# Kernel tuning notes

Hardware: AMD Instinct MI355X
Metric: run time of the kernel (lower is better)

The kernel has to match this reference:

```python
import jax, jax.numpy as jnp
import numpy as np

N_NODES = 100000
N_EDGES = 1600000
N_FEAT = 128
HIDDEN = 128
N_GRAPHS = 64
N_CLASSES = 10
BN_EPS = 1e-5


def setup_inputs() -> dict:
    key = jax.random.key(0)
    ks = jax.random.split(key, 24)
    glorot = lambda k, o, i: jax.random.normal(k, (o, i), jnp.float32) * (1.0 / np.sqrt(i))
    inp = {
        'x': jax.random.normal(ks[0], (N_NODES, N_FEAT), jnp.float32),
        'edge_index': jax.random.randint(ks[1], (2, N_EDGES), 0, N_NODES, jnp.int64),
        'batch': jnp.sort(jax.random.randint(ks[2], (N_NODES,), 0, N_GRAPHS, jnp.int64)),
        # GCNConv(128 -> 128)
        'gcn_w': glorot(ks[3], HIDDEN, N_FEAT),
        'gcn_b': jnp.zeros((HIDDEN,), jnp.float32),
        # SAGEConv layers 1, 2: lin_l (aggregated, with bias) + lin_r (root, no bias)
        'sage1_wl': glorot(ks[4], HIDDEN, HIDDEN),
        'sage1_bl': jnp.zeros((HIDDEN,), jnp.float32),
        'sage1_wr': glorot(ks[5], HIDDEN, HIDDEN),
        'sage2_wl': glorot(ks[6], HIDDEN, HIDDEN),
        'sage2_bl': jnp.zeros((HIDDEN,), jnp.float32),
        'sage2_wr': glorot(ks[7], HIDDEN, HIDDEN),
        # ClassifierBase: 128 -> 200 -> 100 -> 50 -> 10
        'clf_w0': glorot(ks[8], 200, HIDDEN), 'clf_b0': jnp.zeros((200,), jnp.float32),
        'clf_w1': glorot(ks[9], 100, 200), 'clf_b1': jnp.zeros((100,), jnp.float32),
        'clf_w2': glorot(ks[10], 50, 100), 'clf_b2': jnp.zeros((50,), jnp.float32),
        'clf_w3': glorot(ks[11], N_CLASSES, 50), 'clf_b3': jnp.zeros((N_CLASSES,), jnp.float32),
        # BatchNorm1d (eval mode, running_mean=0, running_var=1)
        'bn0_g': jnp.ones((200,), jnp.float32), 'bn0_b': jnp.zeros((200,), jnp.float32),
        'bn1_g': jnp.ones((100,), jnp.float32), 'bn1_b': jnp.zeros((100,), jnp.float32),
        'bn2_g': jnp.ones((50,), jnp.float32), 'bn2_b': jnp.zeros((50,), jnp.float32),
    }
    return inp


def _gcn_conv(x, src, dst, W, b):
    # PyG GCNConv: add self loops, symmetric deg^{-1/2} normalization
    xw = x @ W.T                                                  # [N, H]
    ones = jnp.ones(src.shape[0], xw.dtype)
    deg = jax.ops.segment_sum(ones, dst, num_segments=N_NODES) + 1.0  # self loops
    dinv = jax.lax.rsqrt(deg)
    norm = dinv[src] * dinv[dst]                                  # [E]
    out = jax.ops.segment_sum(xw[src] * norm[:, None], dst, num_segments=N_NODES)
    out = out + xw * (dinv * dinv)[:, None]                       # self-loop term deg^{-1}
    return out + b


def _sage_conv(x, src, dst, Wl, bl, Wr):
    # PyG SAGEConv (mean aggr): lin_l(mean_{j->i} x_j) + lin_r(x_i)
    ones = jnp.ones(src.shape[0], x.dtype)
    cnt = jax.ops.segment_sum(ones, dst, num_segments=N_NODES)
    agg = jax.ops.segment_sum(x[src], dst, num_segments=N_NODES)
    agg = agg / jnp.maximum(cnt, 1.0)[:, None]
    return agg @ Wl.T + bl + x @ Wr.T


def _bn_eval(h, g, b):
    # eval-mode BatchNorm1d with running_mean=0, running_var=1
    return h * (g / np.sqrt(1.0 + BN_EPS)) + b


def reference(x, edge_index, batch, gcn_w, gcn_b,
              sage1_wl, sage1_bl, sage1_wr, sage2_wl, sage2_bl, sage2_wr,
              clf_w0, clf_b0, clf_w1, clf_b1, clf_w2, clf_b2, clf_w3, clf_b3,
              bn0_g, bn0_b, bn1_g, bn1_b, bn2_g, bn2_b):
    src, dst = edge_index[0], edge_index[1]
    h = _gcn_conv(x, src, dst, gcn_w, gcn_b)          # act_func is None -> no activation
    h = _sage_conv(h, src, dst, sage1_wl, sage1_bl, sage1_wr)
    h = _sage_conv(h, src, dst, sage2_wl, sage2_bl, sage2_wr)
    # global mean pool over graphs
    gcnt = jax.ops.segment_sum(jnp.ones(h.shape[0], h.dtype), batch, num_segments=N_GRAPHS)
    g = jax.ops.segment_sum(h, batch, num_segments=N_GRAPHS) / jnp.maximum(gcnt, 1.0)[:, None]
    # ClassifierBase (eval: dropout inactive), tanh activation
    g = jnp.tanh(_bn_eval(g @ clf_w0.T + clf_b0, bn0_g, bn0_b))
    g = jnp.tanh(_bn_eval(g @ clf_w1.T + clf_b1, bn1_g, bn1_b))
    g = jnp.tanh(_bn_eval(g @ clf_w2.T + clf_b2, bn2_g, bn2_b))
    logits = g @ clf_w3.T + clf_b3
    return jax.nn.softmax(logits, axis=1)             # [B, n_classes]
```

## Files before the change

### kernel.cpp

```cpp
#include <hip/hip_runtime.h>

#define N_NODES 100000
#define N_EDGES 1600000
#define NGRAPH 64
#define NBIN 391
#define EPB 6400
#define NBLK 250
#define CAPB 6144
#define CAP 8192
#define PSPLIT 8

typedef short s8v __attribute__((ext_vector_type(8)));
typedef float f4v __attribute__((ext_vector_type(4)));

__device__ __forceinline__ float bflo(unsigned u) { return __uint_as_float(u << 16); }
__device__ __forceinline__ float bfhi(unsigned u) { return __uint_as_float(u & 0xffff0000u); }
__device__ __forceinline__ unsigned short f2bf(float f) {
    unsigned u = __float_as_uint(f);
    u += 0x7fffu + ((u >> 16) & 1u);
    return (unsigned short)(u >> 16);
}
__device__ __forceinline__ float bf2f(unsigned short h) { return __uint_as_float(((unsigned)h) << 16); }
__device__ __forceinline__ unsigned pk(float lo, float hi) {
    return (unsigned)f2bf(lo) | ((unsigned)f2bf(hi) << 16);
}
__device__ __forceinline__ float ldv(const void* p, int i, int f32) {
    return f32 ? ((const float*)p)[i] : bf2f(((const unsigned short*)p)[i]);
}

__global__ void k_detect(const unsigned short* __restrict__ x, const int* __restrict__ ei,
                         const int* __restrict__ batch, int* __restrict__ flags) {
    __shared__ int cnt[3];
    int tid = threadIdx.x;
    if (tid < 3) cnt[tid] = 0;
    __syncthreads();
    unsigned short h = x[tid * 37];
    int e = (h >> 7) & 0xFF;
    if (e >= 100 && e <= 150) atomicAdd(&cnt[0], 1);
    if (ei[2 * (tid * 5000) + 1] == 0) atomicAdd(&cnt[1], 1);
    if (batch[2 * (tid * 193) + 1] == 0) atomicAdd(&cnt[2], 1);
    __syncthreads();
    if (tid == 0) {
        flags[0] = (cnt[0] == 256) ? 0 : 1;
        flags[1] = (cnt[1] == 256) ? 1 : 0;
        flags[2] = (cnt[2] == 256) ? 1 : 0;
    }
}


__global__ void k_bininit(int* __restrict__ binCur) {
    int i = blockIdx.x * 256 + threadIdx.x;
    if (i < NBIN) binCur[i] = i * CAPB;
}

__global__ __launch_bounds__(256) void k_binfill(const int* __restrict__ ei,
                                                 int* __restrict__ binCur,
                                                 unsigned* __restrict__ staging,
                                                 const int* __restrict__ flags) {
    __shared__ int cnt[NBIN];
    __shared__ int lofs[NBIN];
    __shared__ int curL[NBIN];
    __shared__ int basg[NBIN];
    __shared__ int sA[512], sB[512];
    __shared__ unsigned ebuf[EPB];
    int tid = threadIdx.x;
    int i64 = flags[1];
    int base = blockIdx.x * EPB;
    for (int i = tid; i < NBIN; i += 256) cnt[i] = 0;
    __syncthreads();
    for (int k = 0; k < EPB / 256; ++k) {
        int e = base + k * 256 + tid;
        int d = i64 ? ei[2 * (N_EDGES + e)] : ei[N_EDGES + e];
        if ((unsigned)d < N_NODES) atomicAdd(&cnt[d >> 8], 1);
    }
    __syncthreads();
    for (int k = tid; k < 512; k += 256) sA[k] = (k < NBIN) ? cnt[k] : 0;
    __syncthreads();
    int* src = sA;
    int* dst = sB;
    for (int off = 1; off < 512; off <<= 1) {
        for (int k = tid; k < 512; k += 256)
            dst[k] = src[k] + ((k >= off) ? src[k - off] : 0);
        __syncthreads();
        int* t = src; src = dst; dst = t;
    }
    for (int i = tid; i < NBIN; i += 256) {
        int excl = src[i] - cnt[i];
        lofs[i] = excl;
        curL[i] = excl;
        basg[i] = cnt[i] ? atomicAdd(&binCur[i], cnt[i]) : 0;
    }
    __syncthreads();
    for (int k = 0; k < EPB / 256; ++k) {
        int e = base + k * 256 + tid;
        int s = i64 ? ei[2 * e] : ei[e];
        int d = i64 ? ei[2 * (N_EDGES + e)] : ei[N_EDGES + e];
        if ((unsigned)d < N_NODES) {
            s = min(max(s, 0), N_NODES - 1);
            int p = atomicAdd(&curL[d >> 8], 1);
            ebuf[p] = ((unsigned)(d & 255) << 20) | (unsigned)s;
        }
    }
    __syncthreads();
    int wid = tid >> 6, lane = tid & 63;
    for (int b = wid; b < NBIN; b += 4) {
        int n = cnt[b], lo = lofs[b], go = basg[b];
        int cap = (b + 1) * CAPB;
        for (int l = lane; l < n; l += 64)
            if (go + l < cap) staging[go + l] = ebuf[lo + l];
    }
}

__global__ __launch_bounds__(256) void k_csr(const unsigned* __restrict__ staging,
                                             const int* __restrict__ binCur,
                                             int* __restrict__ rsA, int* __restrict__ reA,
                                             float* __restrict__ dinv,
                                             int* __restrict__ colidx) {
    __shared__ int deg[256];
    __shared__ int s[256];
    __shared__ int cur[256];
    __shared__ unsigned ebuf[CAP];
    __shared__ int colbuf[CAP];
    int b = blockIdx.x, tid = threadIdx.x;
    int n0 = b << 8;
    int nend = min(256, N_NODES - n0);
    int runStart = b * CAPB;
    int runLen = min(binCur[b] - runStart, CAPB);
    deg[tid] = 0;
    __syncthreads();
    for (int i = tid; i < runLen; i += 256) {
        unsigned e = staging[runStart + i];
        ebuf[i] = e;
        atomicAdd(&deg[e >> 20], 1);
    }
    __syncthreads();
    int myDeg = deg[tid];
    s[tid] = myDeg;
    __syncthreads();
    for (int off = 1; off < 256; off <<= 1) {
        int x = (tid >= off) ? s[tid - off] : 0;
        __syncthreads();
        s[tid] += x;
        __syncthreads();
    }
    int incl = s[tid];
    if (tid < nend) {
        rsA[n0 + tid] = runStart + incl - myDeg;
        reA[n0 + tid] = runStart + incl;
        dinv[n0 + tid] = rsqrtf((float)myDeg + 1.0f);
    }
    cur[tid] = incl - myDeg;
    __syncthreads();
    for (int i = tid; i < runLen; i += 256) {
        unsigned e = ebuf[i];
        int p = atomicAdd(&cur[e >> 20], 1);
        colbuf[p] = (int)(e & 0xFFFFF);
    }
    __syncthreads();
    for (int i = tid; i < runLen; i += 256) colidx[runStart + i] = colbuf[i];
}

__global__ void k_gb(const int* __restrict__ batch, int* __restrict__ gstart,
                     const int* __restrict__ flags) {
    int g = threadIdx.x;
    if (g > NGRAPH) return;
    int b64 = flags[2];
    int lo = 0, hi = N_NODES;
    while (lo < hi) {
        int mid = (lo + hi) >> 1;
        int v = b64 ? batch[2 * mid] : batch[mid];
        if (v < g) lo = mid + 1;
        else hi = mid;
    }
    gstart[g] = lo;
}

__global__ __launch_bounds__(256) void k_prescale(const void* __restrict__ src,
                                                  const float* __restrict__ dinv,
                                                  unsigned* __restrict__ out,
                                                  const int* __restrict__ flags) {
    int id = blockIdx.x * 256 + threadIdx.x;
    int node = id >> 6;
    float di = dinv[node];
    float lo, hi;
    if (flags[0]) {
        float2 u = ((const float2*)src)[id];
        lo = u.x; hi = u.y;
    } else {
        unsigned u = ((const unsigned*)src)[id];
        lo = bflo(u); hi = bfhi(u);
    }
    out[id] = pk(di * lo, di * hi);
}

__global__ __launch_bounds__(256) void k_agg(const uint4* __restrict__ xs,
                                             const int* __restrict__ rsA,
                                             const int* __restrict__ reA,
                                             const float* __restrict__ dinv,
                                             unsigned* __restrict__ out, int mode,
                                             const int* __restrict__ col) {
    int lane = threadIdx.x & 63;
    int node = blockIdx.x * 4 + (threadIdx.x >> 6);
    int glane = lane & 15, grp = lane >> 4;
    int rs = rsA[node], re = reA[node];
    int deg = re - rs;
    float a[8];
    #pragma unroll
    for (int i = 0; i < 8; ++i) a[i] = 0.f;
    uint4 selfu = make_uint4(0u, 0u, 0u, 0u);
    if (mode == 0) selfu = xs[(size_t)node * 16 + glane];

    int efull = rs + (deg & ~15);
    for (int base = rs; base < efull; base += 16) {
        int j0 = col[base + grp * 4 + 0];
        int j1 = col[base + grp * 4 + 1];
        int j2 = col[base + grp * 4 + 2];
        int j3 = col[base + grp * 4 + 3];
        uint4 u0 = xs[(size_t)j0 * 16 + glane];
        uint4 u1 = xs[(size_t)j1 * 16 + glane];
        uint4 u2 = xs[(size_t)j2 * 16 + glane];
        uint4 u3 = xs[(size_t)j3 * 16 + glane];
        a[0] += bflo(u0.x) + bflo(u1.x) + bflo(u2.x) + bflo(u3.x);
        a[1] += bfhi(u0.x) + bfhi(u1.x) + bfhi(u2.x) + bfhi(u3.x);
        a[2] += bflo(u0.y) + bflo(u1.y) + bflo(u2.y) + bflo(u3.y);
        a[3] += bfhi(u0.y) + bfhi(u1.y) + bfhi(u2.y) + bfhi(u3.y);
        a[4] += bflo(u0.z) + bflo(u1.z) + bflo(u2.z) + bflo(u3.z);
        a[5] += bfhi(u0.z) + bfhi(u1.z) + bfhi(u2.z) + bfhi(u3.z);
        a[6] += bflo(u0.w) + bflo(u1.w) + bflo(u2.w) + bflo(u3.w);
        a[7] += bfhi(u0.w) + bfhi(u1.w) + bfhi(u2.w) + bfhi(u3.w);
    }
    if (efull < re) {
        int j[4];
        float w[4];
        #pragma unroll
        for (int k = 0; k < 4; ++k) {
            int ee = efull + grp * 4 + k;
            bool v = ee < re;
            j[k] = col[v ? ee : re - 1];
            w[k] = v ? 1.f : 0.f;
        }
        uint4 u0 = xs[(size_t)j[0] * 16 + glane];
        uint4 u1 = xs[(size_t)j[1] * 16 + glane];
        uint4 u2 = xs[(size_t)j[2] * 16 + glane];
        uint4 u3 = xs[(size_t)j[3] * 16 + glane];
        a[0] += w[0] * bflo(u0.x) + w[1] * bflo(u1.x) + w[2] * bflo(u2.x) + w[3] * bflo(u3.x);
        a[1] += w[0] * bfhi(u0.x) + w[1] * bfhi(u1.x) + w[2] * bfhi(u2.x) + w[3] * bfhi(u3.x);
        a[2] += w[0] * bflo(u0.y) + w[1] * bflo(u1.y) + w[2] * bflo(u2.y) + w[3] * bflo(u3.y);
        a[3] += w[0] * bfhi(u0.y) + w[1] * bfhi(u1.y) + w[2] * bfhi(u2.y) + w[3] * bfhi(u3.y);
        a[4] += w[0] * bflo(u0.z) + w[1] * bflo(u1.z) + w[2] * bflo(u2.z) + w[3] * bflo(u3.z);
        a[5] += w[0] * bfhi(u0.z) + w[1] * bfhi(u1.z) + w[2] * bfhi(u2.z) + w[3] * bfhi(u3.z);
        a[6] += w[0] * bflo(u0.w) + w[1] * bflo(u1.w) + w[2] * bflo(u2.w) + w[3] * bflo(u3.w);
        a[7] += w[0] * bfhi(u0.w) + w[1] * bfhi(u1.w) + w[2] * bfhi(u2.w) + w[3] * bfhi(u3.w);
    }
    #pragma unroll
    for (int i = 0; i < 8; ++i) {
        float v = a[i];
        v += __shfl_xor(v, 16, 64);
        v += __shfl_xor(v, 32, 64);
        a[i] = v;
    }
    if (mode == 0) {
        float di = dinv[node];
        a[0] = di * (a[0] + bflo(selfu.x)); a[1] = di * (a[1] + bfhi(selfu.x));
        a[2] = di * (a[2] + bflo(selfu.y)); a[3] = di * (a[3] + bfhi(selfu.y));
        a[4] = di * (a[4] + bflo(selfu.z)); a[5] = di * (a[5] + bfhi(selfu.z));
        a[6] = di * (a[6] + bflo(selfu.w)); a[7] = di * (a[7] + bfhi(selfu.w));
    } else {
        float s = 1.0f / fmaxf((float)deg, 1.0f);
        #pragma unroll
        for (int i = 0; i < 8; ++i) a[i] *= s;
    }
    if (grp == 0) {
        uint4 o;
        o.x = pk(a[0], a[1]); o.y = pk(a[2], a[3]);
        o.z = pk(a[4], a[5]); o.w = pk(a[6], a[7]);
        *(uint4*)(out + (size_t)node * 64 + glane * 4) = o;
    }
}

template <int DUAL>
__global__ __launch_bounds__(256) void k_gemm(const unsigned short* A0,
                                              const void* __restrict__ W0,
                                              const unsigned short* __restrict__ A1,
                                              const void* __restrict__ W1,
                                              const void* __restrict__ bias,
                                              unsigned short* out,
                                              const int* __restrict__ flags) {
    __shared__ __align__(16) unsigned short As[64][136];
    __shared__ __align__(16) unsigned short Ws[128][136];
    int f32 = flags[0];
    int tid = threadIdx.x;
    int lane = tid & 63;
    int rowbase = blockIdx.x * 64;
    int lr = lane & 15, q = lane >> 4;
    int m0 = (tid >> 6) * 16;

    f4v acc[8];
    #pragma unroll
    for (int t = 0; t < 8; ++t) acc[t] = (f4v){0.f, 0.f, 0.f, 0.f};

    #pragma unroll
    for (int p = 0; p < (DUAL ? 2 : 1); ++p) {
        const unsigned short* Ap = p ? A1 : A0;
        const void* Wp = p ? W1 : W0;
        if (p) __syncthreads();
        #pragma unroll
        for (int it = 0; it < 4; ++it) {
            int chunk = tid + it * 256;
            int r = chunk >> 4, c8 = (chunk & 15) * 8;
            int grow = rowbase + r;
            uint4 v = make_uint4(0u, 0u, 0u, 0u);
            if (grow < N_NODES) v = *(const uint4*)(Ap + (size_t)grow * 128 + c8);
            *(uint4*)&As[r][c8] = v;
        }
        if (!f32) {
            const unsigned short* Wf = (const unsigned short*)Wp;
            #pragma unroll
            for (int it = 0; it < 8; ++it) {
                int chunk = tid + it * 256;
                int r = chunk >> 4, c8 = (chunk & 15) * 8;
                *(uint4*)&Ws[r][c8] = *(const uint4*)(Wf + r * 128 + c8);
            }
        } else {
            const float* Wf = (const float*)Wp;
            #pragma unroll
            for (int it = 0; it < 16; ++it) {
                int chunk = tid + it * 256;
                int r = chunk >> 5, c4 = (chunk & 31) * 4;
                float4 v = *(const float4*)(Wf + r * 128 + c4);
                unsigned lo = (unsigned)f2bf(v.x) | ((unsigned)f2bf(v.y) << 16);
                unsigned hi = (unsigned)f2bf(v.z) | ((unsigned)f2bf(v.w) << 16);
                *(uint2*)&Ws[r][c4] = make_uint2(lo, hi);
            }
        }
        __syncthreads();
        #pragma unroll
        for (int k = 0; k < 4; ++k) {
            s8v a = *(const s8v*)&As[m0 + lr][k * 32 + q * 8];
            #pragma unroll
            for (int t = 0; t < 8; ++t) {
                s8v b = *(const s8v*)&Ws[t * 16 + lr][k * 32 + q * 8];
                acc[t] = __builtin_amdgcn_mfma_f32_16x16x32_bf16(a, b, acc[t], 0, 0, 0);
            }
        }
    }
    #pragma unroll
    for (int t = 0; t < 8; ++t) {
        int o = t * 16 + lr;
        float bv = ldv(bias, o, f32);
        #pragma unroll
        for (int j = 0; j < 4; ++j) {
            int m = rowbase + m0 + q * 4 + j;
            if (m < N_NODES) out[(size_t)m * 128 + o] = f2bf(acc[t][j] + bv);
        }
    }
}

__global__ __launch_bounds__(256) void k_pool2(const unsigned* __restrict__ h,
                                               const int* __restrict__ gstart,
                                               float* __restrict__ ppool) {
    __shared__ float part[4][128];
    int g = blockIdx.x / PSPLIT, sl = blockIdx.x % PSPLIT;
    int wave = threadIdx.x >> 6, lane = threadIdx.x & 63;
    int s0 = gstart[g], s1 = gstart[g + 1];
    int n = s1 - s0;
    int chunk = (n + PSPLIT - 1) / PSPLIT;
    int r0 = s0 + sl * chunk;
    int r1 = min(r0 + chunk, s1);
    float a0 = 0.f, a1 = 0.f;
    for (int r = r0 + wave; r < r1; r += 4) {
        unsigned u = h[(size_t)r * 64 + lane];
        a0 += bflo(u);
        a1 += bfhi(u);
    }
    part[wave][2 * lane] = a0;
    part[wave][2 * lane + 1] = a1;
    __syncthreads();
    int t = threadIdx.x;
    if (t < 128) {
        float s = part[0][t] + part[1][t] + part[2][t] + part[3][t];
        ppool[(size_t)blockIdx.x * 128 + t] = s;
    }
}

__global__ void k_cvt_w(const void* w0, const void* w1, const void* w2, const void* w3,
                        float* __restrict__ wbuf, const int* __restrict__ flags) {
    int f = flags[0];
    int i = blockIdx.x * 256 + threadIdx.x;
    if (i < 25600) wbuf[i] = ldv(w0, i, f);
    else if (i < 45600) wbuf[i] = ldv(w1, i - 25600, f);
    else if (i < 50600) wbuf[i] = ldv(w2, i - 45600, f);
    else if (i < 51100) wbuf[i] = ldv(w3, i - 50600, f);
}

__global__ void k_cvt_p(const void* b0, const void* bn0g, const void* bn0b,
                        const void* b1, const void* bn1g, const void* bn1b,
                        const void* b2, const void* bn2g, const void* bn2b,
                        const void* b3, float* __restrict__ pbuf,
                        const int* __restrict__ flags) {
    int f = flags[0];
    int t = threadIdx.x;
    const float invs = rsqrtf(1.0f + 1e-5f);
    if (t < 200) {
        float a = ldv(bn0g, t, f) * invs;
        pbuf[t] = a;
        pbuf[200 + t] = ldv(b0, t, f) * a + ldv(bn0b, t, f);
    }
    if (t < 100) {
        float a = ldv(bn1g, t, f) * invs;
        pbuf[400 + t] = a;
        pbuf[500 + t] = ldv(b1, t, f) * a + ldv(bn1b, t, f);
    }
    if (t < 50) {
        float a = ldv(bn2g, t, f) * invs;
        pbuf[600 + t] = a;
        pbuf[650 + t] = ldv(b2, t, f) * a + ldv(bn2b, t, f);
    }
    if (t < 10) pbuf[700 + t] = ldv(b3, t, f);
}

__global__ __launch_bounds__(256) void k_clf0(const float* __restrict__ ppool,
                                              const int* __restrict__ gstart,
                                              const float* __restrict__ wbuf,
                                              const float* __restrict__ pbuf,
                                              float* __restrict__ h1) {
    __shared__ float g[128];
    int b = blockIdx.x, t = threadIdx.x;
    if (t < 128) {
        float s = 0.f;
        #pragma unroll
        for (int k = 0; k < PSPLIT; ++k) s += ppool[(size_t)(b * PSPLIT + k) * 128 + t];
        int cnt = gstart[b + 1] - gstart[b];
        g[t] = s / fmaxf((float)cnt, 1.0f);
    }
    __syncthreads();
    if (t < 200) {
        const float4* wr = (const float4*)(wbuf + t * 128);
        float s = 0.f;
        #pragma unroll
        for (int k = 0; k < 32; ++k) {
            float4 v = wr[k];
            s += v.x * g[4 * k] + v.y * g[4 * k + 1] + v.z * g[4 * k + 2] + v.w * g[4 * k + 3];
        }
        h1[b * 200 + t] = tanhf(s * pbuf[t] + pbuf[200 + t]);
    }
}

__global__ __launch_bounds__(128) void k_clf1(const float* __restrict__ h1,
                                              const float* __restrict__ wbuf,
                                              const float* __restrict__ pbuf,
                                              float* __restrict__ h2) {
    __shared__ float g[200];
    int b = blockIdx.x, t = threadIdx.x;
    for (int i = t; i < 200; i += 128) g[i] = h1[b * 200 + i];
    __syncthreads();
    if (t < 100) {
        const float4* wr = (const float4*)(wbuf + 25600 + t * 200);
        float s = 0.f;
        #pragma unroll
        for (int k = 0; k < 50; ++k) {
            float4 v = wr[k];
            s += v.x * g[4 * k] + v.y * g[4 * k + 1] + v.z * g[4 * k + 2] + v.w * g[4 * k + 3];
        }
        h2[b * 100 + t] = tanhf(s * pbuf[400 + t] + pbuf[500 + t]);
    }
}

__global__ __launch_bounds__(128) void k_clf2(const float* __restrict__ h2,
                                              const float* __restrict__ wbuf,
                                              const float* __restrict__ pbuf,
                                              float* __restrict__ h3) {
    __shared__ float g[100];
    int b = blockIdx.x, t = threadIdx.x;
    if (t < 100) g[t] = h2[b * 100 + t];
    __syncthreads();
    if (t < 50) {
        const float4* wr = (const float4*)(wbuf + 45600 + t * 100);
        float s = 0.f;
        #pragma unroll
        for (int k = 0; k < 25; ++k) {
            float4 v = wr[k];
            s += v.x * g[4 * k] + v.y * g[4 * k + 1] + v.z * g[4 * k + 2] + v.w * g[4 * k + 3];
        }
        h3[b * 50 + t] = tanhf(s * pbuf[600 + t] + pbuf[650 + t]);
    }
}

__global__ __launch_bounds__(64) void k_clf3(const float* __restrict__ h3,
                                             const float* __restrict__ wbuf,
                                             const float* __restrict__ pbuf,
                                             void* outv, const int* __restrict__ flags) {
    int b = threadIdx.x;
    int f = flags[0];
    const float* h = h3 + b * 50;
    float lg[10];
    float mx = -1e30f;
    #pragma unroll
    for (int c = 0; c < 10; ++c) {
        const float* wr = wbuf + 50600 + c * 50;
        float s = 0.f;
        for (int k = 0; k < 50; ++k) s += wr[k] * h[k];
        s += pbuf[700 + c];
        lg[c] = s;
        mx = fmaxf(mx, s);
    }
    float sum = 0.f;
    #pragma unroll
    for (int c = 0; c < 10; ++c) {
        lg[c] = __expf(lg[c] - mx);
        sum += lg[c];
    }
    float inv = 1.0f / sum;
    #pragma unroll
    for (int c = 0; c < 10; ++c) {
        float v = lg[c] * inv;
        if (f) ((float*)outv)[b * 10 + c] = v;
        else ((unsigned short*)outv)[b * 10 + c] = f2bf(v);
    }
}

extern "C" void kernel_launch(void* const* d_in, const int* in_sizes, int n_in,
                              void* d_out, int out_size, void* d_ws, size_t ws_size,
                              hipStream_t stream) {
    const unsigned short* x16 = (const unsigned short*)d_in[0];
    const int* ei = (const int*)d_in[1];
    const int* batch = (const int*)d_in[2];

    char* ws = (char*)d_ws;
    size_t off = 0;
    auto alloc = [&](size_t bytes) {
        size_t r = off;
        off = (off + bytes + 255) & ~(size_t)255;
        return r;
    };
    int* flags = (int*)(ws + alloc(256));
    int* rsA = (int*)(ws + alloc((size_t)N_NODES * 4));
    int* reA = (int*)(ws + alloc((size_t)N_NODES * 4));
    int* colidx = (int*)(ws + alloc((size_t)NBIN * CAPB * 4));
    float* dinv = (float*)(ws + alloc((size_t)N_NODES * 4));
    int* binCur = (int*)(ws + alloc(NBIN * 4));
    int* gstart = (int*)(ws + alloc((NGRAPH + 1) * 4));
    float* ppool = (float*)(ws + alloc((size_t)NGRAPH * PSPLIT * 128 * 4));
    float* wbuf = (float*)(ws + alloc(51100 * 4));
    float* pbuf = (float*)(ws + alloc(710 * 4));
    float* h1 = (float*)(ws + alloc(64 * 200 * 4));
    float* h2 = (float*)(ws + alloc(64 * 100 * 4));
    float* h3 = (float*)(ws + alloc(64 * 50 * 4));
    unsigned short* bufA = (unsigned short*)(ws + alloc((size_t)N_NODES * 128 * 2));
    unsigned short* bufB = (unsigned short*)(ws + alloc((size_t)N_NODES * 128 * 2));
    unsigned* staging = (unsigned*)bufA;

    k_detect<<<1, 256, 0, stream>>>(x16, ei, batch, flags);
    k_bininit<<<(NBIN + 255) / 256, 256, 0, stream>>>(binCur);

    k_cvt_w<<<200, 256, 0, stream>>>(d_in[11], d_in[13], d_in[15], d_in[17], wbuf, flags);
    k_cvt_p<<<1, 256, 0, stream>>>(d_in[12], d_in[19], d_in[20], d_in[14], d_in[21], d_in[22],
                                   d_in[16], d_in[23], d_in[24], d_in[18], pbuf, flags);
    k_gb<<<1, 128, 0, stream>>>(batch, gstart, flags);

    k_binfill<<<NBLK, 256, 0, stream>>>(ei, binCur, staging, flags);
    k_csr<<<NBIN, 256, 0, stream>>>(staging, binCur, rsA, reA, dinv, colidx);

    k_prescale<<<N_NODES * 64 / 256, 256, 0, stream>>>((const void*)x16, dinv,
                                                       (unsigned*)bufB, flags);
    k_agg<<<N_NODES / 4, 256, 0, stream>>>((const uint4*)bufB, rsA, reA, dinv,
                                           (unsigned*)bufA, 0, colidx);
    k_gemm<0><<<(N_NODES + 63) / 64, 256, 0, stream>>>(bufA, d_in[3], nullptr, nullptr, d_in[4],
                                                       bufA, flags);
    k_agg<<<N_NODES / 4, 256, 0, stream>>>((const uint4*)bufA, rsA, reA, dinv,
                                           (unsigned*)bufB, 1, colidx);
    k_gemm<1><<<(N_NODES + 63) / 64, 256, 0, stream>>>(bufB, d_in[5], bufA, d_in[7], d_in[6],
                                                       bufB, flags);
    k_agg<<<N_NODES / 4, 256, 0, stream>>>((const uint4*)bufB, rsA, reA, dinv,
                                           (unsigned*)bufA, 1, colidx);
    k_gemm<1><<<(N_NODES + 63) / 64, 256, 0, stream>>>(bufA, d_in[8], bufB, d_in[10], d_in[9],
                                                       bufA, flags);
    k_pool2<<<NGRAPH * PSPLIT, 256, 0, stream>>>((const unsigned*)bufA, gstart, ppool);
    k_clf0<<<NGRAPH, 256, 0, stream>>>(ppool, gstart, wbuf, pbuf, h1);
    k_clf1<<<NGRAPH, 128, 0, stream>>>(h1, wbuf, pbuf, h2);
    k_clf2<<<NGRAPH, 128, 0, stream>>>(h2, wbuf, pbuf, h3);
    k_clf3<<<1, 64, 0, stream>>>(h3, wbuf, pbuf, d_out, flags);
}
```

Before: 524.4 us.

## Fuse setup kernels, fold prescale into CSR, merge pooling with classifier

Result: slower. 568.9 us (+8.5%).

```diff
diff --git a/kernel.cpp b/kernel.cpp
--- a/kernel.cpp
+++ b/kernel.cpp
@@ -28,8 +28,17 @@
     return f32 ? ((const float*)p)[i] : bf2f(((const unsigned short*)p)[i]);
 }
 
-__global__ void k_detect(const unsigned short* __restrict__ x, const int* __restrict__ ei,
-                         const int* __restrict__ batch, int* __restrict__ flags) {
+__global__ __launch_bounds__(256) void k_setup(const unsigned short* __restrict__ x,
+                                               const int* __restrict__ ei,
+                                               const int* __restrict__ batch,
+                                               int* __restrict__ flags,
+                                               int* __restrict__ binCur,
+                                               int* __restrict__ gstart,
+                                               float* __restrict__ pbuf,
+                                               const void* b0, const void* bn0g, const void* bn0b,
+                                               const void* b1, const void* bn1g, const void* bn1b,
+                                               const void* b2, const void* bn2g, const void* bn2b,
+                                               const void* b3) {
     __shared__ int cnt[3];
     int tid = threadIdx.x;
     if (tid < 3) cnt[tid] = 0;
@@ -40,17 +49,41 @@
     if (ei[2 * (tid * 5000) + 1] == 0) atomicAdd(&cnt[1], 1);
     if (batch[2 * (tid * 193) + 1] == 0) atomicAdd(&cnt[2], 1);
     __syncthreads();
+    int f = (cnt[0] == 256) ? 0 : 1;
+    int b64 = (cnt[2] == 256) ? 1 : 0;
     if (tid == 0) {
-        flags[0] = (cnt[0] == 256) ? 0 : 1;
+        flags[0] = f;
         flags[1] = (cnt[1] == 256) ? 1 : 0;
-        flags[2] = (cnt[2] == 256) ? 1 : 0;
-    }
-}
-
-
-__global__ void k_bininit(int* __restrict__ binCur) {
-    int i = blockIdx.x * 256 + threadIdx.x;
-    if (i < NBIN) binCur[i] = i * CAPB;
+        flags[2] = b64;
+    }
+    for (int i = tid; i < NBIN; i += 256) binCur[i] = i * CAPB;
+    if (tid <= NGRAPH) {
+        int g = tid, lo = 0, hi = N_NODES;
+        while (lo < hi) {
+            int mid = (lo + hi) >> 1;
+            int v = b64 ? batch[2 * mid] : batch[mid];
+            if (v < g) lo = mid + 1;
+            else hi = mid;
+        }
+        gstart[g] = lo;
+    }
+    const float invs = rsqrtf(1.0f + 1e-5f);
+    if (tid < 200) {
+        float a = ldv(bn0g, tid, f) * invs;
+        pbuf[tid] = a;
+        pbuf[200 + tid] = ldv(b0, tid, f) * a + ldv(bn0b, tid, f);
+    }
+    if (tid < 100) {
+        float a = ldv(bn1g, tid, f) * invs;
+        pbuf[400 + tid] = a;
+        pbuf[500 + tid] = ldv(b1, tid, f) * a + ldv(bn1b, tid, f);
+    }
+    if (tid < 50) {
+        float a = ldv(bn2g, tid, f) * invs;
+        pbuf[600 + tid] = a;
+        pbuf[650 + tid] = ldv(b2, tid, f) * a + ldv(bn2b, tid, f);
+    }
+    if (tid < 10) pbuf[700 + tid] = ldv(b3, tid, f);
 }
 
 __global__ __launch_bounds__(256) void k_binfill(const int* __restrict__ ei,
@@ -115,7 +148,10 @@
                                              const int* __restrict__ binCur,
                                              int* __restrict__ rsA, int* __restrict__ reA,
                                              float* __restrict__ dinv,
-                                             int* __restrict__ colidx) {
+                                             int* __restrict__ colidx,
+                                             const void* __restrict__ x,
+                                             unsigned* __restrict__ ybuf,
+                                             const int* __restrict__ flags) {
     __shared__ int deg[256];
     __shared__ int s[256];
     __shared__ int cur[256];
@@ -138,9 +174,9 @@
     s[tid] = myDeg;
     __syncthreads();
     for (int off = 1; off < 256; off <<= 1) {
-        int x = (tid >= off) ? s[tid - off] : 0;
+        int x2 = (tid >= off) ? s[tid - off] : 0;
         __syncthreads();
-        s[tid] += x;
+        s[tid] += x2;
         __syncthreads();
     }
     int incl = s[tid];
@@ -158,39 +194,24 @@
     }
     __syncthreads();
     for (int i = tid; i < runLen; i += 256) colidx[runStart + i] = colbuf[i];
-}
-
-__global__ void k_gb(const int* __restrict__ batch, int* __restrict__ gstart,
-                     const int* __restrict__ flags) {
-    int g = threadIdx.x;
-    if (g > NGRAPH) return;
-    int b64 = flags[2];
-    int lo = 0, hi = N_NODES;
-    while (lo < hi) {
-        int mid = (lo + hi) >> 1;
-        int v = b64 ? batch[2 * mid] : batch[mid];
-        if (v < g) lo = mid + 1;
-        else hi = mid;
-    }
-    gstart[g] = lo;
-}
-
-__global__ __launch_bounds__(256) void k_prescale(const void* __restrict__ src,
-                                                  const float* __restrict__ dinv,
-                                                  unsigned* __restrict__ out,
-                                                  const int* __restrict__ flags) {
-    int id = blockIdx.x * 256 + threadIdx.x;
-    int node = id >> 6;
-    float di = dinv[node];
-    float lo, hi;
-    if (flags[0]) {
-        float2 u = ((const float2*)src)[id];
-        lo = u.x; hi = u.y;
-    } else {
-        unsigned u = ((const unsigned*)src)[id];
-        lo = bflo(u); hi = bfhi(u);
-    }
-    out[id] = pk(di * lo, di * hi);
+    int f32 = flags[0];
+    int prow = tid >> 6, ppair = tid & 63;
+    for (int it = 0; it < 64; ++it) {
+        int rl = it * 4 + prow;
+        int r = n0 + rl;
+        if (r < N_NODES) {
+            float di = rsqrtf((float)deg[rl] + 1.0f);
+            float lo, hi;
+            if (f32) {
+                float2 u = ((const float2*)x)[(size_t)r * 64 + ppair];
+                lo = u.x; hi = u.y;
+            } else {
+                unsigned u = ((const unsigned*)x)[(size_t)r * 64 + ppair];
+                lo = bflo(u); hi = bfhi(u);
+            }
+            ybuf[(size_t)r * 64 + ppair] = pk(di * lo, di * hi);
+        }
+    }
 }
 
 __global__ __launch_bounds__(256) void k_agg(const uint4* __restrict__ xs,
@@ -356,166 +377,137 @@
     }
 }
 
-__global__ __launch_bounds__(256) void k_pool2(const unsigned* __restrict__ h,
-                                               const int* __restrict__ gstart,
-                                               float* __restrict__ ppool) {
-    __shared__ float part[4][128];
-    int g = blockIdx.x / PSPLIT, sl = blockIdx.x % PSPLIT;
-    int wave = threadIdx.x >> 6, lane = threadIdx.x & 63;
+__global__ __launch_bounds__(512) void k_poolclf(const unsigned* __restrict__ h,
+                                                 const int* __restrict__ gstart,
+                                                 const float* __restrict__ pbuf,
+                                                 const void* w0, const void* w1,
+                                                 const void* w2, const void* w3,
+                                                 void* outv, const int* __restrict__ flags) {
+    __shared__ float part[8][128];
+    __shared__ float gmean[128];
+    __shared__ float h1s[200];
+    __shared__ float h2s[100];
+    __shared__ float h3s[50];
+    __shared__ float lg[10];
+    int g = blockIdx.x, t = threadIdx.x;
+    int wave = t >> 6, lane = t & 63;
+    int f = flags[0];
     int s0 = gstart[g], s1 = gstart[g + 1];
-    int n = s1 - s0;
-    int chunk = (n + PSPLIT - 1) / PSPLIT;
-    int r0 = s0 + sl * chunk;
-    int r1 = min(r0 + chunk, s1);
     float a0 = 0.f, a1 = 0.f;
-    for (int r = r0 + wave; r < r1; r += 4) {
-        unsigned u = h[(size_t)r * 64 + lane];
-        a0 += bflo(u);
-        a1 += bfhi(u);
+    for (int r = s0 + wave * 4; r < s1; r += 32) {
+        #pragma unroll
+        for (int k = 0; k < 4; ++k) {
+            int rr = r + k;
+            if (rr < s1) {
+                unsigned u = h[(size_t)rr * 64 + lane];
+                a0 += bflo(u);
+                a1 += bfhi(u);
+            }
+        }
     }
     part[wave][2 * lane] = a0;
     part[wave][2 * lane + 1] = a1;
     __syncthreads();
-    int t = threadIdx.x;
-    if (t < 128) {
-        float s = part[0][t] + part[1][t] + part[2][t] + part[3][t];
-        ppool[(size_t)blockIdx.x * 128 + t] = s;
-    }
-}
-
-__global__ void k_cvt_w(const void* w0, const void* w1, const void* w2, const void* w3,
-                        float* __restrict__ wbuf, const int* __restrict__ flags) {
-    int f = flags[0];
-    int i = blockIdx.x * 256 + threadIdx.x;
-    if (i < 25600) wbuf[i] = ldv(w0, i, f);
-    else if (i < 45600) wbuf[i] = ldv(w1, i - 25600, f);
-    else if (i < 50600) wbuf[i] = ldv(w2, i - 45600, f);
-    else if (i < 51100) wbuf[i] = ldv(w3, i - 50600, f);
-}
-
-__global__ void k_cvt_p(const void* b0, const void* bn0g, const void* bn0b,
-                        const void* b1, const void* bn1g, const void* bn1b,
-                        const void* b2, const void* bn2g, const void* bn2b,
-                        const void* b3, float* __restrict__ pbuf,
-                        const int* __restrict__ flags) {
-    int f = flags[0];
-    int t = threadIdx.x;
-    const float invs = rsqrtf(1.0f + 1e-5f);
-    if (t < 200) {
-        float a = ldv(bn0g, t, f) * invs;
-        pbuf[t] = a;
-        pbuf[200 + t] = ldv(b0, t, f) * a + ldv(bn0b, t, f);
-    }
-    if (t < 100) {
-        float a = ldv(bn1g, t, f) * invs;
-        pbuf[400 + t] = a;
-        pbuf[500 + t] = ldv(b1, t, f) * a + ldv(bn1b, t, f);
-    }
-    if (t < 50) {
-        float a = ldv(bn2g, t, f) * invs;
-        pbuf[600 + t] = a;
-        pbuf[650 + t] = ldv(b2, t, f) * a + ldv(bn2b, t, f);
-    }
-    if (t < 10) pbuf[700 + t] = ldv(b3, t, f);
-}
-
-__global__ __launch_bounds__(256) void k_clf0(const float* __restrict__ ppool,
-                                              const int* __restrict__ gstart,
-                                              const float* __restrict__ wbuf,
-                                              const float* __restrict__ pbuf,
-                                              float* __restrict__ h1) {
-    __shared__ float g[128];
-    int b = blockIdx.x, t = threadIdx.x;
     if (t < 128) {
         float s = 0.f;
         #pragma unroll
-        for (int k = 0; k < PSPLIT; ++k) s += ppool[(size_t)(b * PSPLIT + k) * 128 + t];
-        int cnt = gstart[b + 1] - gstart[b];
-        g[t] = s / fmaxf((float)cnt, 1.0f);
+        for (int k = 0; k < 8; ++k) s += part[k][t];
+        gmean[t] = s / fmaxf((float)(s1 - s0), 1.0f);
     }
     __syncthreads();
     if (t < 200) {
-        const float4* wr = (const float4*)(wbuf + t * 128);
         float s = 0.f;
-        #pragma unroll
-        for (int k = 0; k < 32; ++k) {
-            float4 v = wr[k];
-            s += v.x * g[4 * k] + v.y * g[4 * k + 1] + v.z * g[4 * k + 2] + v.w * g[4 * k + 3];
-        }
-        h1[b * 200 + t] = tanhf(s * pbuf[t] + pbuf[200 + t]);
-    }
-}
-
-__global__ __launch_bounds__(128) void k_clf1(const float* __restrict__ h1,
-                                              const float* __restrict__ wbuf,
-                                              const float* __restrict__ pbuf,
-                                              float* __restrict__ h2) {
-    __shared__ float g[200];
-    int b = blockIdx.x, t = threadIdx.x;
-    for (int i = t; i < 200; i += 128) g[i] = h1[b * 200 + i];
+        if (f) {
+            const float4* wr = (const float4*)w0 + t * 32;
+            #pragma unroll
+            for (int k = 0; k < 32; ++k) {
+                float4 v = wr[k];
+                s += v.x * gmean[4 * k] + v.y * gmean[4 * k + 1] +
+                     v.z * gmean[4 * k + 2] + v.w * gmean[4 * k + 3];
+            }
+        } else {
+            const unsigned* wr = (const unsigned*)w0 + t * 64;
+            for (int k = 0; k < 64; ++k) {
+                unsigned u = wr[k];
+                s += bflo(u) * gmean[2 * k] + bfhi(u) * gmean[2 * k + 1];
+            }
+        }
+        h1s[t] = tanhf(s * pbuf[t] + pbuf[200 + t]);
+    }
     __syncthreads();
     if (t < 100) {
-        const float4* wr = (const float4*)(wbuf + 25600 + t * 200);
         float s = 0.f;
-        #pragma unroll
-        for (int k = 0; k < 50; ++k) {
-            float4 v = wr[k];
-            s += v.x * g[4 * k] + v.y * g[4 * k + 1] + v.z * g[4 * k + 2] + v.w * g[4 * k + 3];
-        }
-        h2[b * 100 + t] = tanhf(s * pbuf[400 + t] + pbuf[500 + t]);
-    }
-}
-
-__global__ __launch_bounds__(128) void k_clf2(const float* __restrict__ h2,
-                                              const float* __restrict__ wbuf,
-                                              const float* __restrict__ pbuf,
-                                              float* __restrict__ h3) {
-    __shared__ float g[100];
-    int b = blockIdx.x, t = threadIdx.x;
-    if (t < 100) g[t] = h2[b * 100 + t];
+        if (f) {
+            const float4* wr = (const float4*)w1 + t * 50;
+            #pragma unroll
+            for (int k = 0; k < 50; ++k) {
+                float4 v = wr[k];
+                s += v.x * h1s[4 * k] + v.y * h1s[4 * k + 1] +
+                     v.z * h1s[4 * k + 2] + v.w * h1s[4 * k + 3];
+            }
+        } else {
+            const unsigned* wr = (const unsigned*)w1 + t * 100;
+            for (int k = 0; k < 100; ++k) {
+                unsigned u = wr[k];
+                s += bflo(u) * h1s[2 * k] + bfhi(u) * h1s[2 * k + 1];
+            }
+        }
+        h2s[t] = tanhf(s * pbuf[400 + t] + pbuf[500 + t]);
+    }
     __syncthreads();
     if (t < 50) {
-        const float4* wr = (const float4*)(wbuf + 45600 + t * 100);
         float s = 0.f;
-        #pragma unroll
-        for (int k = 0; k < 25; ++k) {
-            float4 v = wr[k];
-            s += v.x * g[4 * k] + v.y * g[4 * k + 1] + v.z * g[4 * k + 2] + v.w * g[4 * k + 3];
-        }
-        h3[b * 50 + t] = tanhf(s * pbuf[600 + t] + pbuf[650 + t]);
-    }
-}
-
-__global__ __launch_bounds__(64) void k_clf3(const float* __restrict__ h3,
-                                             const float* __restrict__ wbuf,
-                                             const float* __restrict__ pbuf,
-                                             void* outv, const int* __restrict__ flags) {
-    int b = threadIdx.x;
-    int f = flags[0];
-    const float* h = h3 + b * 50;
-    float lg[10];
-    float mx = -1e30f;
-    #pragma unroll
-    for (int c = 0; c < 10; ++c) {
-        const float* wr = wbuf + 50600 + c * 50;
+        if (f) {
+            const float4* wr = (const float4*)w2 + t * 25;
+            #pragma unroll
+            for (int k = 0; k < 25; ++k) {
+                float4 v = wr[k];
+                s += v.x * h2s[4 * k] + v.y * h2s[4 * k + 1] +
+                     v.z * h2s[4 * k + 2] + v.w * h2s[4 * k + 3];
+            }
+        } else {
+            const unsigned* wr = (const unsigned*)w2 + t * 50;
+            for (int k = 0; k < 50; ++k) {
+                unsigned u = wr[k];
+                s += bflo(u) * h2s[2 * k] + bfhi(u) * h2s[2 * k + 1];
+            }
+        }
+        h3s[t] = tanhf(s * pbuf[600 + t] + pbuf[650 + t]);
+    }
+    __syncthreads();
+    if (t < 10) {
         float s = 0.f;
-        for (int k = 0; k < 50; ++k) s += wr[k] * h[k];
-        s += pbuf[700 + c];
-        lg[c] = s;
-        mx = fmaxf(mx, s);
-    }
-    float sum = 0.f;
-    #pragma unroll
-    for (int c = 0; c < 10; ++c) {
-        lg[c] = __expf(lg[c] - mx);
-        sum += lg[c];
-    }
-    float inv = 1.0f / sum;
-    #pragma unroll
-    for (int c = 0; c < 10; ++c) {
-        float v = lg[c] * inv;
-        if (f) ((float*)outv)[b * 10 + c] = v;
-        else ((unsigned short*)outv)[b * 10 + c] = f2bf(v);
+        if (f) {
+            const float* wr = (const float*)w3 + t * 50;
+            for (int k = 0; k < 50; ++k) s += wr[k] * h3s[k];
+        } else {
+            const unsigned* wr = (const unsigned*)((const unsigned short*)w3 + t * 50);
+            for (int k = 0; k < 25; ++k) {
+                unsigned u = wr[k];
+                s += bflo(u) * h3s[2 * k] + bfhi(u) * h3s[2 * k + 1];
+            }
+        }
+        lg[t] = s + pbuf[700 + t];
+    }
+    __syncthreads();
+    if (t == 0) {
+        float mx = -1e30f;
+        #pragma unroll
+        for (int c = 0; c < 10; ++c) mx = fmaxf(mx, lg[c]);
+        float sum = 0.f;
+        float ex[10];
+        #pragma unroll
+        for (int c = 0; c < 10; ++c) {
+            ex[c] = __expf(lg[c] - mx);
+            sum += ex[c];
+        }
+        float inv = 1.0f / sum;
+        #pragma unroll
+        for (int c = 0; c < 10; ++c) {
+            float v = ex[c] * inv;
+            if (f) ((float*)outv)[g * 10 + c] = v;
+            else ((unsigned short*)outv)[g * 10 + c] = f2bf(v);
+        }
     }
 }
 
@@ -540,29 +532,20 @@
     float* dinv = (float*)(ws + alloc((size_t)N_NODES * 4));
     int* binCur = (int*)(ws + alloc(NBIN * 4));
     int* gstart = (int*)(ws + alloc((NGRAPH + 1) * 4));
-    float* ppool = (float*)(ws + alloc((size_t)NGRAPH * PSPLIT * 128 * 4));
-    float* wbuf = (float*)(ws + alloc(51100 * 4));
     float* pbuf = (float*)(ws + alloc(710 * 4));
-    float* h1 = (float*)(ws + alloc(64 * 200 * 4));
-    float* h2 = (float*)(ws + alloc(64 * 100 * 4));
-    float* h3 = (float*)(ws + alloc(64 * 50 * 4));
     unsigned short* bufA = (unsigned short*)(ws + alloc((size_t)N_NODES * 128 * 2));
     unsigned short* bufB = (unsigned short*)(ws + alloc((size_t)N_NODES * 128 * 2));
     unsigned* staging = (unsigned*)bufA;
 
-    k_detect<<<1, 256, 0, stream>>>(x16, ei, batch, flags);
-    k_bininit<<<(NBIN + 255) / 256, 256, 0, stream>>>(binCur);
-
-    k_cvt_w<<<200, 256, 0, stream>>>(d_in[11], d_in[13], d_in[15], d_in[17], wbuf, flags);
-    k_cvt_p<<<1, 256, 0, stream>>>(d_in[12], d_in[19], d_in[20], d_in[14], d_in[21], d_in[22],
-                                   d_in[16], d_in[23], d_in[24], d_in[18], pbuf, flags);
-    k_gb<<<1, 128, 0, stream>>>(batch, gstart, flags);
+    k_setup<<<1, 256, 0, stream>>>(x16, ei, batch, flags, binCur, gstart, pbuf,
+                                   d_in[12], d_in[19], d_in[20],
+                                   d_in[14], d_in[21], d_in[22],
+                                   d_in[16], d_in[23], d_in[24], d_in[18]);
 
     k_binfill<<<NBLK, 256, 0, stream>>>(ei, binCur, staging, flags);
-    k_csr<<<NBIN, 256, 0, stream>>>(staging, binCur, rsA, reA, dinv, colidx);
-
-    k_prescale<<<N_NODES * 64 / 256, 256, 0, stream>>>((const void*)x16, dinv,
-                                                       (unsigned*)bufB, flags);
+    k_csr<<<NBIN, 256, 0, stream>>>(staging, binCur, rsA, reA, dinv, colidx,
+                                    (const void*)x16, (unsigned*)bufB, flags);
+
     k_agg<<<N_NODES / 4, 256, 0, stream>>>((const uint4*)bufB, rsA, reA, dinv,
                                            (unsigned*)bufA, 0, colidx);
     k_gemm<0><<<(N_NODES + 63) / 64, 256, 0, stream>>>(bufA, d_in[3], nullptr, nullptr, d_in[4],
@@ -575,9 +558,7 @@
                                            (unsigned*)bufA, 1, colidx);
     k_gemm<1><<<(N_NODES + 63) / 64, 256, 0, stream>>>(bufA, d_in[8], bufB, d_in[10], d_in[9],
                                                        bufA, flags);
-    k_pool2<<<NGRAPH * PSPLIT, 256, 0, stream>>>((const unsigned*)bufA, gstart, ppool);
-    k_clf0<<<NGRAPH, 256, 0, stream>>>(ppool, gstart, wbuf, pbuf, h1);
-    k_clf1<<<NGRAPH, 128, 0, stream>>>(h1, wbuf, pbuf, h2);
-    k_clf2<<<NGRAPH, 128, 0, stream>>>(h2, wbuf, pbuf, h3);
-    k_clf3<<<1, 64, 0, stream>>>(h3, wbuf, pbuf, d_out, flags);
-}
+    k_poolclf<<<NGRAPH, 512, 0, stream>>>((const unsigned*)bufA, gstart, pbuf,
+                                          d_in[11], d_in[13], d_in[15], d_in[17],
+                                          d_out, flags);
+}
```
